# Performance work log

Measured on AMD Instinct MI355X. Metric: run time of the kernel, lower is better.

## Reference

```python
import jax, jax.numpy as jnp
import numpy as np


def _xavier(key, shape):
    fan_out, fan_in = shape[0], shape[1]
    lim = np.sqrt(6.0 / (fan_in + fan_out)).astype(np.float32)
    return jax.random.uniform(key, shape, jnp.float32, -lim, lim)


def setup_inputs() -> dict:
    key = jax.random.key(0)
    ks = jax.random.split(key, 28)
    B, D, G, ND = 16384, 32, 6, 8
    V_user, V_item, V_gender, V_age, V_occ, V_genre = 1000000, 100000, 2, 7, 21, 19
    H1, H2 = 128, 64
    deep_in = 6 * D + ND  # 200
    return {
        "user_id": jax.random.randint(ks[0], (B,), 0, V_user),
        "item_id": jax.random.randint(ks[1], (B,), 0, V_item),
        "user_gender": jax.random.randint(ks[2], (B,), 0, V_gender),
        "user_age": jax.random.randint(ks[3], (B,), 0, V_age),
        "user_occupation": jax.random.randint(ks[4], (B,), 0, V_occ),
        "item_genre_ids": jax.random.randint(ks[5], (B, G), 0, V_genre),
        "item_genre_mask": jax.random.randint(ks[6], (B, G), 0, 2).astype(jnp.float32),
        "dense_features": jax.random.normal(ks[7], (B, ND), jnp.float32),
        # first-order (1-dim) embedding tables
        "fo_user": _xavier(ks[8], (V_user, 1)),
        "fo_item": _xavier(ks[9], (V_item, 1)),
        "fo_gender": _xavier(ks[10], (V_gender, 1)),
        "fo_age": _xavier(ks[11], (V_age, 1)),
        "fo_occ": _xavier(ks[12], (V_occ, 1)),
        "fo_genre": _xavier(ks[13], (V_genre, 1)),
        # second-order / deep embedding tables
        "emb_user": _xavier(ks[14], (V_user, D)),
        "emb_item": _xavier(ks[15], (V_item, D)),
        "emb_gender": _xavier(ks[16], (V_gender, D)),
        "emb_age": _xavier(ks[17], (V_age, D)),
        "emb_occ": _xavier(ks[18], (V_occ, D)),
        "emb_genre": _xavier(ks[19], (V_genre, D)),
        # dense linear + deep MLP
        "dense_W": _xavier(ks[20], (1, ND)),
        "dense_b": jnp.zeros((1,), jnp.float32),
        "W1": _xavier(ks[21], (H1, deep_in)),
        "b1": jnp.zeros((H1,), jnp.float32),
        "W2": _xavier(ks[22], (H2, H1)),
        "b2": jnp.zeros((H2,), jnp.float32),
        "Wout": _xavier(ks[23], (1, H2)),
        "bout": jnp.zeros((1,), jnp.float32),
    }


def _pool(table, ids, mask):
    # masked mean-pool over the genre list axis
    e = table[ids]                       # [B, G, d]
    m = mask[..., None]                  # [B, G, 1]
    denom = jnp.clip(m.sum(axis=1), 1.0)  # [B, 1]
    return (e * m).sum(axis=1) / denom   # [B, d]


def reference(user_id, item_id, user_gender, user_age, user_occupation,
              item_genre_ids, item_genre_mask, dense_features,
              fo_user, fo_item, fo_gender, fo_age, fo_occ, fo_genre,
              emb_user, emb_item, emb_gender, emb_age, emb_occ, emb_genre,
              dense_W, dense_b, W1, b1, W2, b2, Wout, bout):
    # FM first order: sum of 1-dim gathers + pooled genre + dense linear -> [B,1]
    first = (fo_user[user_id] + fo_item[item_id] + fo_gender[user_gender]
             + fo_age[user_age] + fo_occ[user_occupation]
             + _pool(fo_genre, item_genre_ids, item_genre_mask)
             + dense_features @ dense_W.T + dense_b)
    # FM second order: stack field embeddings [B, 6, D]
    x = jnp.stack([emb_user[user_id], emb_item[item_id], emb_gender[user_gender],
                   emb_age[user_age], emb_occ[user_occupation],
                   _pool(emb_genre, item_genre_ids, item_genre_mask)], axis=1)
    s = x.sum(axis=1)                                   # [B, D]
    second = 0.5 * (s * s - (x * x).sum(axis=1)).sum(axis=1, keepdims=True)  # [B,1]
    # deep part (dropout is identity in eval mode)
    deep_in = jnp.concatenate([x.reshape(x.shape[0], -1), dense_features], axis=1)
    h = jax.nn.relu(deep_in @ W1.T + b1)
    h = jax.nn.relu(h @ W2.T + b2)
    deep = h @ Wout.T + bout                            # [B,1]
    return (first + second + deep).squeeze(1)           # [B]
```

## Files before the change

### kernel.cpp

```cpp
#include <hip/hip_runtime.h>


typedef float v2f __attribute__((ext_vector_type(2)));
static __device__ __forceinline__ v2f bc2(float x) { v2f r; r.x = x; r.y = x; return r; }
static __device__ __forceinline__ float relu1(float x) { return fmaxf(x, 0.f); }

#define ROWS_PER_BLOCK 16
#define ROWS_PER_WAVE 4
#define DI_STRIDE 204
#define H1_STRIDE 132

__global__ void pack_weights(const float* __restrict__ W1, const float* __restrict__ W2,
                             float4* __restrict__ W1p, float4* __restrict__ W2p) {
    const int idx = blockIdx.x * blockDim.x + threadIdx.x;
    if (idx < 6400) {
        const int s = idx & 1, jp = (idx >> 1) & 15, k4 = (idx >> 5) % 50, w = idx / 1600;
        const int j0 = w * 32 + 2 * jp, c = 4 * k4 + 2 * s;
        W1p[idx] = make_float4(W1[j0 * 200 + c],     W1[(j0 + 1) * 200 + c],
                               W1[j0 * 200 + c + 1], W1[(j0 + 1) * 200 + c + 1]);
    }
    if (idx < 2048) {
        const int s = idx & 1, jp = (idx >> 1) & 7, k4 = (idx >> 4) & 31, w = idx >> 9;
        const int j0 = w * 16 + 2 * jp, c = 4 * k4 + 2 * s;
        W2p[idx] = make_float4(W2[j0 * 128 + c],     W2[(j0 + 1) * 128 + c],
                               W2[j0 * 128 + c + 1], W2[(j0 + 1) * 128 + c + 1]);
    }
}

__global__ __launch_bounds__(256) void deepfm_kernel(
    const int* __restrict__ user_id, const int* __restrict__ item_id,
    const int* __restrict__ gender_, const int* __restrict__ age_,
    const int* __restrict__ occ_, const int* __restrict__ genre_ids,
    const float* __restrict__ genre_mask, const float* __restrict__ dense,
    const float* __restrict__ fo_user, const float* __restrict__ fo_item,
    const float* __restrict__ fo_gender, const float* __restrict__ fo_age,
    const float* __restrict__ fo_occ, const float* __restrict__ fo_genre,
    const float* __restrict__ emb_user, const float* __restrict__ emb_item,
    const float* __restrict__ emb_gender, const float* __restrict__ emb_age,
    const float* __restrict__ emb_occ, const float* __restrict__ emb_genre,
    const float* __restrict__ dense_W, const float* __restrict__ dense_b,
    const float4* __restrict__ W1p, const float* __restrict__ b1,
    const float4* __restrict__ W2p, const float* __restrict__ b2,
    const float* __restrict__ Wout, const float* __restrict__ bout,
    float* __restrict__ out, int B)
{
    __shared__ float lds_di[ROWS_PER_BLOCK][DI_STRIDE];
    __shared__ float lds_rs[ROWS_PER_BLOCK];
    __shared__ float lds_part[ROWS_PER_BLOCK][4];

    const int tid = threadIdx.x;
    const int wid = tid >> 6;
    const int lane = tid & 63;
    const int blockRow0 = blockIdx.x * ROWS_PER_BLOCK;

    {
        const int rowBase = blockRow0 + wid * ROWS_PER_WAVE;
        int uid[ROWS_PER_WAVE], iid[ROWS_PER_WAVE], gg[ROWS_PER_WAVE],
            aa[ROWS_PER_WAVE], oo[ROWS_PER_WAVE];
        #pragma unroll
        for (int r = 0; r < ROWS_PER_WAVE; ++r) {
            int row = rowBase + r; if (row >= B) row = B - 1;
            uid[r] = user_id[row]; iid[r] = item_id[row];
            gg[r] = gender_[row];  aa[r] = age_[row];  oo[r] = occ_[row];
        }

        #pragma unroll
        for (int r = 0; r < ROWS_PER_WAVE; ++r) {
            int row = rowBase + r; if (row >= B) row = B - 1;
            const int ri = wid * ROWS_PER_WAVE + r;

            int gid[6]; float mk[6]; float msum = 0.f;
            #pragma unroll
            for (int t = 0; t < 6; ++t) {
                gid[t] = genre_ids[row * 6 + t];
                mk[t]  = genre_mask[row * 6 + t];
                msum  += mk[t];
            }
            const float inv_den = 1.0f / fmaxf(msum, 1.0f);

            float pe_sum = 0.f, pe_sq = 0.f;
            {
                float v = (lane < 32) ? emb_user[(size_t)uid[r] * 32 + lane]
                                      : emb_item[(size_t)iid[r] * 32 + (lane - 32)];
                lds_di[ri][lane] = v;
                pe_sum += v; pe_sq += v * v;
            }
            {
                float v = (lane < 32) ? emb_gender[gg[r] * 32 + lane]
                                      : emb_age[aa[r] * 32 + (lane - 32)];
                lds_di[ri][64 + lane] = v;
                pe_sum += v; pe_sq += v * v;
            }
            {
                float v;
                if (lane < 32) {
                    v = emb_occ[oo[r] * 32 + lane];
                } else {
                    const int d = lane - 32;
                    float s = 0.f;
                    #pragma unroll
                    for (int t = 0; t < 6; ++t) s += mk[t] * emb_genre[gid[t] * 32 + d];
                    v = s * inv_den;
                }
                lds_di[ri][128 + lane] = v;
                pe_sum += v; pe_sq += v * v;
            }
            if (lane < 8) lds_di[ri][192 + lane] = dense[(size_t)row * 8 + lane];

            float s2 = pe_sum + __shfl_xor(pe_sum, 32);
            float ss = pe_sq  + __shfl_xor(pe_sq, 32);
            float t2 = 0.5f * (s2 * s2 - ss);
            #pragma unroll
            for (int off = 16; off >= 1; off >>= 1) t2 += __shfl_xor(t2, off);

            float fo = fo_user[uid[r]] + fo_item[iid[r]] + fo_gender[gg[r]]
                     + fo_age[aa[r]] + fo_occ[oo[r]];
            float fg = 0.f;
            #pragma unroll
            for (int t = 0; t < 6; ++t) fg += mk[t] * fo_genre[gid[t]];
            fo += fg * inv_den;
            float dd = 0.f;
            #pragma unroll
            for (int j = 0; j < 8; ++j) dd += dense[(size_t)row * 8 + j] * dense_W[j];
            fo += dd + dense_b[0];

            if (lane == 0) lds_rs[ri] = fo + t2;
        }
    }
    __syncthreads();

    const int jp1 = lane & 15;
    const int rh  = lane >> 4;

    v2f acc[ROWS_PER_WAVE];
    #pragma unroll
    for (int r = 0; r < ROWS_PER_WAVE; ++r) acc[r] = bc2(0.f);

    {
        const float4* __restrict__ W1b = W1p + wid * 1600;
        const float4* __restrict__ dv = reinterpret_cast<const float4*>(&lds_di[0][0]);

        for (int k4 = 0; k4 < 50; ++k4) {
            const float4 wa = W1b[(k4 * 16 + jp1) * 2 + 0];
            const float4 wb = W1b[(k4 * 16 + jp1) * 2 + 1];
            const v2f w0 = { wa.x, wa.y }, w1 = { wa.z, wa.w };
            const v2f w2 = { wb.x, wb.y }, w3 = { wb.z, wb.w };
            #pragma unroll
            for (int r = 0; r < ROWS_PER_WAVE; ++r) {
                const float4 a = dv[(rh + 4 * r) * 51 + k4];
                acc[r] = __builtin_elementwise_fma(w0, bc2(a.x), acc[r]);
                acc[r] = __builtin_elementwise_fma(w1, bc2(a.y), acc[r]);
                acc[r] = __builtin_elementwise_fma(w2, bc2(a.z), acc[r]);
                acc[r] = __builtin_elementwise_fma(w3, bc2(a.w), acc[r]);
            }
        }
    }
    __syncthreads();

    float* __restrict__ h1b = &lds_di[0][0];
    {
        const int j0 = wid * 32 + 2 * jp1;
        const float2 bb = *reinterpret_cast<const float2*>(b1 + j0);
        #pragma unroll
        for (int r = 0; r < ROWS_PER_WAVE; ++r) {
            const int row = rh + 4 * r;
            reinterpret_cast<float2*>(h1b)[(row * H1_STRIDE + j0) >> 1] =
                make_float2(relu1(acc[r].x + bb.x), relu1(acc[r].y + bb.y));
        }
    }
    __syncthreads();

    const int jp2 = lane & 7;
    const int rh2 = lane >> 3;

    v2f acc2[2];
    acc2[0] = bc2(0.f); acc2[1] = bc2(0.f);

    {
        const float4* __restrict__ W2b = W2p + wid * 512;
        const float4* __restrict__ h1v = reinterpret_cast<const float4*>(h1b);

        for (int k4 = 0; k4 < 32; ++k4) {
            const float4 wa = W2b[(k4 * 8 + jp2) * 2 + 0];
            const float4 wb = W2b[(k4 * 8 + jp2) * 2 + 1];
            const v2f w0 = { wa.x, wa.y }, w1 = { wa.z, wa.w };
            const v2f w2 = { wb.x, wb.y }, w3 = { wb.z, wb.w };
            #pragma unroll
            for (int t = 0; t < 2; ++t) {
                const float4 h = h1v[(rh2 + 8 * t) * 33 + k4];
                acc2[t] = __builtin_elementwise_fma(w0, bc2(h.x), acc2[t]);
                acc2[t] = __builtin_elementwise_fma(w1, bc2(h.y), acc2[t]);
                acc2[t] = __builtin_elementwise_fma(w2, bc2(h.z), acc2[t]);
                acc2[t] = __builtin_elementwise_fma(w3, bc2(h.w), acc2[t]);
            }
        }
    }

    {
        const int j0 = wid * 16 + 2 * jp2;
        const float2 bb2 = *reinterpret_cast<const float2*>(b2 + j0);
        const float2 wo  = *reinterpret_cast<const float2*>(Wout + j0);
        #pragma unroll
        for (int t = 0; t < 2; ++t) {
            const float h2x = relu1(acc2[t].x + bb2.x);
            const float h2y = relu1(acc2[t].y + bb2.y);
            float v = wo.x * h2x + wo.y * h2y;
            v += __shfl_xor(v, 1); v += __shfl_xor(v, 2); v += __shfl_xor(v, 4);
            if (jp2 == 0) lds_part[rh2 + 8 * t][wid] = v;
        }
    }
    __syncthreads();

    if (tid < ROWS_PER_BLOCK) {
        const int row = blockRow0 + tid;
        if (row < B) {
            const float deep = lds_part[tid][0] + lds_part[tid][1]
                             + lds_part[tid][2] + lds_part[tid][3] + bout[0];
            out[row] = deep + lds_rs[tid];
        }
    }
}

extern "C" void kernel_launch(void* const* d_in, const int* in_sizes, int n_in,
                              void* d_out, int out_size, void* d_ws, size_t ws_size,
                              hipStream_t stream) {
    const int B = in_sizes[0];

    float4* W1p = reinterpret_cast<float4*>(d_ws);
    float4* W2p = reinterpret_cast<float4*>((char*)d_ws + 102400);

    pack_weights<<<25, 256, 0, stream>>>(
        (const float*)d_in[22], (const float*)d_in[24], W1p, W2p);

    const int grid = (B + ROWS_PER_BLOCK - 1) / ROWS_PER_BLOCK;
    deepfm_kernel<<<grid, 256, 0, stream>>>(
        (const int*)d_in[0],  (const int*)d_in[1],  (const int*)d_in[2],
        (const int*)d_in[3],  (const int*)d_in[4],  (const int*)d_in[5],
        (const float*)d_in[6],  (const float*)d_in[7],
        (const float*)d_in[8],  (const float*)d_in[9],  (const float*)d_in[10],
        (const float*)d_in[11], (const float*)d_in[12], (const float*)d_in[13],
        (const float*)d_in[14], (const float*)d_in[15], (const float*)d_in[16],
        (const float*)d_in[17], (const float*)d_in[18], (const float*)d_in[19],
        (const float*)d_in[20], (const float*)d_in[21],
        W1p, (const float*)d_in[23],
        W2p, (const float*)d_in[25],
        (const float*)d_in[26], (const float*)d_in[27],
        (float*)d_out, B);
}
```

Before: 296.1 us.

## Split fused DeepFM kernel into gather/FM kernel and MLP kernel via global scratch

Splits the single fused kernel into a gather+FM kernel (two rows per wave, writing the 200-wide deep input and the FM scalar to workspace) and a separate MLP kernel that reads the deep input directly from global memory instead of LDS. The aim is to decouple latency-bound random embedding gathers from the compute-bound MLP so each runs with better occupancy and parallelism. The cost is an extra global round trip of about 13 MB, plus one more launch, and the MLP now reads its activations through uncoalesced global float4 loads rather than LDS. The MLP loops also gain unroll-2 pragmas.

New measurement: 274.8 us. -7.2%, faster.

```diff
diff --git a/kernel.cpp b/kernel.cpp
--- a/kernel.cpp
+++ b/kernel.cpp
@@ -5,9 +5,6 @@
 static __device__ __forceinline__ v2f bc2(float x) { v2f r; r.x = x; r.y = x; return r; }
 static __device__ __forceinline__ float relu1(float x) { return fmaxf(x, 0.f); }
 
-#define ROWS_PER_BLOCK 16
-#define ROWS_PER_WAVE 4
-#define DI_STRIDE 204
 #define H1_STRIDE 132
 
 __global__ void pack_weights(const float* __restrict__ W1, const float* __restrict__ W2,
@@ -27,7 +24,7 @@
     }
 }
 
-__global__ __launch_bounds__(256) void deepfm_kernel(
+__global__ __launch_bounds__(256) void gather_fm_kernel(
     const int* __restrict__ user_id, const int* __restrict__ item_id,
     const int* __restrict__ gender_, const int* __restrict__ age_,
     const int* __restrict__ occ_, const int* __restrict__ genre_ids,
@@ -39,115 +36,108 @@
     const float* __restrict__ emb_gender, const float* __restrict__ emb_age,
     const float* __restrict__ emb_occ, const float* __restrict__ emb_genre,
     const float* __restrict__ dense_W, const float* __restrict__ dense_b,
+    float* __restrict__ di, float* __restrict__ rs, int B)
+{
+    const int tid = threadIdx.x;
+    const int wid = tid >> 6;
+    const int lane = tid & 63;
+    const int waveG = blockIdx.x * 4 + wid;
+    const int d = lane & 31;
+
+    #pragma unroll
+    for (int r = 0; r < 2; ++r) {
+        int row = waveG * 2 + r; if (row >= B) row = B - 1;
+
+        const int uid = user_id[row], iid = item_id[row];
+        const int gg = gender_[row], aa = age_[row], oo = occ_[row];
+
+        int gid[6]; float mk[6]; float msum = 0.f;
+        #pragma unroll
+        for (int t = 0; t < 6; ++t) {
+            gid[t] = genre_ids[row * 6 + t];
+            mk[t]  = genre_mask[row * 6 + t];
+            msum  += mk[t];
+        }
+        const float inv_den = 1.0f / fmaxf(msum, 1.0f);
+
+        const float v0 = (lane < 32) ? emb_user[(size_t)uid * 32 + d]
+                                     : emb_item[(size_t)iid * 32 + d];
+        const float v1 = (lane < 32) ? emb_gender[gg * 32 + d]
+                                     : emb_age[aa * 32 + d];
+        float v2;
+        if (lane < 32) {
+            v2 = emb_occ[oo * 32 + d];
+        } else {
+            float s = 0.f;
+            #pragma unroll
+            for (int t = 0; t < 6; ++t) s += mk[t] * emb_genre[gid[t] * 32 + d];
+            v2 = s * inv_den;
+        }
+
+        float* __restrict__ dro = di + (size_t)row * 200;
+        dro[lane] = v0;
+        dro[64 + lane] = v1;
+        dro[128 + lane] = v2;
+        if (lane < 8) dro[192 + lane] = dense[(size_t)row * 8 + lane];
+
+        const float pe_sum = v0 + v1 + v2;
+        const float pe_sq  = v0 * v0 + v1 * v1 + v2 * v2;
+        const float s2 = pe_sum + __shfl_xor(pe_sum, 32);
+        const float ss = pe_sq  + __shfl_xor(pe_sq, 32);
+        float t2 = 0.5f * (s2 * s2 - ss);
+        #pragma unroll
+        for (int off = 16; off >= 1; off >>= 1) t2 += __shfl_xor(t2, off);
+
+        float fo = fo_user[uid] + fo_item[iid] + fo_gender[gg]
+                 + fo_age[aa] + fo_occ[oo];
+        float fg = 0.f;
+        #pragma unroll
+        for (int t = 0; t < 6; ++t) fg += mk[t] * fo_genre[gid[t]];
+        fo += fg * inv_den;
+        float dd = 0.f;
+        #pragma unroll
+        for (int j = 0; j < 8; ++j) dd += dense[(size_t)row * 8 + j] * dense_W[j];
+        fo += dd + dense_b[0];
+
+        if (lane == 0) rs[row] = fo + t2;
+    }
+}
+
+__global__ __launch_bounds__(256) void mlp_kernel(
     const float4* __restrict__ W1p, const float* __restrict__ b1,
     const float4* __restrict__ W2p, const float* __restrict__ b2,
     const float* __restrict__ Wout, const float* __restrict__ bout,
+    const float* __restrict__ di, const float* __restrict__ rs,
     float* __restrict__ out, int B)
 {
-    __shared__ float lds_di[ROWS_PER_BLOCK][DI_STRIDE];
-    __shared__ float lds_rs[ROWS_PER_BLOCK];
-    __shared__ float lds_part[ROWS_PER_BLOCK][4];
+    __shared__ float h1s[16][H1_STRIDE];
+    __shared__ float lds_part[16][4];
 
     const int tid = threadIdx.x;
     const int wid = tid >> 6;
     const int lane = tid & 63;
-    const int blockRow0 = blockIdx.x * ROWS_PER_BLOCK;
-
-    {
-        const int rowBase = blockRow0 + wid * ROWS_PER_WAVE;
-        int uid[ROWS_PER_WAVE], iid[ROWS_PER_WAVE], gg[ROWS_PER_WAVE],
-            aa[ROWS_PER_WAVE], oo[ROWS_PER_WAVE];
-        #pragma unroll
-        for (int r = 0; r < ROWS_PER_WAVE; ++r) {
-            int row = rowBase + r; if (row >= B) row = B - 1;
-            uid[r] = user_id[row]; iid[r] = item_id[row];
-            gg[r] = gender_[row];  aa[r] = age_[row];  oo[r] = occ_[row];
-        }
-
-        #pragma unroll
-        for (int r = 0; r < ROWS_PER_WAVE; ++r) {
-            int row = rowBase + r; if (row >= B) row = B - 1;
-            const int ri = wid * ROWS_PER_WAVE + r;
-
-            int gid[6]; float mk[6]; float msum = 0.f;
-            #pragma unroll
-            for (int t = 0; t < 6; ++t) {
-                gid[t] = genre_ids[row * 6 + t];
-                mk[t]  = genre_mask[row * 6 + t];
-                msum  += mk[t];
-            }
-            const float inv_den = 1.0f / fmaxf(msum, 1.0f);
-
-            float pe_sum = 0.f, pe_sq = 0.f;
-            {
-                float v = (lane < 32) ? emb_user[(size_t)uid[r] * 32 + lane]
-                                      : emb_item[(size_t)iid[r] * 32 + (lane - 32)];
-                lds_di[ri][lane] = v;
-                pe_sum += v; pe_sq += v * v;
-            }
-            {
-                float v = (lane < 32) ? emb_gender[gg[r] * 32 + lane]
-                                      : emb_age[aa[r] * 32 + (lane - 32)];
-                lds_di[ri][64 + lane] = v;
-                pe_sum += v; pe_sq += v * v;
-            }
-            {
-                float v;
-                if (lane < 32) {
-                    v = emb_occ[oo[r] * 32 + lane];
-                } else {
-                    const int d = lane - 32;
-                    float s = 0.f;
-                    #pragma unroll
-                    for (int t = 0; t < 6; ++t) s += mk[t] * emb_genre[gid[t] * 32 + d];
-                    v = s * inv_den;
-                }
-                lds_di[ri][128 + lane] = v;
-                pe_sum += v; pe_sq += v * v;
-            }
-            if (lane < 8) lds_di[ri][192 + lane] = dense[(size_t)row * 8 + lane];
-
-            float s2 = pe_sum + __shfl_xor(pe_sum, 32);
-            float ss = pe_sq  + __shfl_xor(pe_sq, 32);
-            float t2 = 0.5f * (s2 * s2 - ss);
-            #pragma unroll
-            for (int off = 16; off >= 1; off >>= 1) t2 += __shfl_xor(t2, off);
-
-            float fo = fo_user[uid[r]] + fo_item[iid[r]] + fo_gender[gg[r]]
-                     + fo_age[aa[r]] + fo_occ[oo[r]];
-            float fg = 0.f;
-            #pragma unroll
-            for (int t = 0; t < 6; ++t) fg += mk[t] * fo_genre[gid[t]];
-            fo += fg * inv_den;
-            float dd = 0.f;
-            #pragma unroll
-            for (int j = 0; j < 8; ++j) dd += dense[(size_t)row * 8 + j] * dense_W[j];
-            fo += dd + dense_b[0];
-
-            if (lane == 0) lds_rs[ri] = fo + t2;
-        }
-    }
-    __syncthreads();
+    const int row0 = blockIdx.x * 16;
 
     const int jp1 = lane & 15;
     const int rh  = lane >> 4;
 
-    v2f acc[ROWS_PER_WAVE];
+    v2f acc[4];
     #pragma unroll
-    for (int r = 0; r < ROWS_PER_WAVE; ++r) acc[r] = bc2(0.f);
+    for (int r = 0; r < 4; ++r) acc[r] = bc2(0.f);
 
     {
         const float4* __restrict__ W1b = W1p + wid * 1600;
-        const float4* __restrict__ dv = reinterpret_cast<const float4*>(&lds_di[0][0]);
-
+        const float4* __restrict__ dg = reinterpret_cast<const float4*>(di);
+
+        #pragma unroll 2
         for (int k4 = 0; k4 < 50; ++k4) {
             const float4 wa = W1b[(k4 * 16 + jp1) * 2 + 0];
             const float4 wb = W1b[(k4 * 16 + jp1) * 2 + 1];
             const v2f w0 = { wa.x, wa.y }, w1 = { wa.z, wa.w };
             const v2f w2 = { wb.x, wb.y }, w3 = { wb.z, wb.w };
             #pragma unroll
-            for (int r = 0; r < ROWS_PER_WAVE; ++r) {
-                const float4 a = dv[(rh + 4 * r) * 51 + k4];
+            for (int r = 0; r < 4; ++r) {
+                const float4 a = dg[(size_t)(row0 + rh + 4 * r) * 50 + k4];
                 acc[r] = __builtin_elementwise_fma(w0, bc2(a.x), acc[r]);
                 acc[r] = __builtin_elementwise_fma(w1, bc2(a.y), acc[r]);
                 acc[r] = __builtin_elementwise_fma(w2, bc2(a.z), acc[r]);
@@ -155,16 +145,14 @@
             }
         }
     }
-    __syncthreads();
-
-    float* __restrict__ h1b = &lds_di[0][0];
+
     {
         const int j0 = wid * 32 + 2 * jp1;
         const float2 bb = *reinterpret_cast<const float2*>(b1 + j0);
         #pragma unroll
-        for (int r = 0; r < ROWS_PER_WAVE; ++r) {
+        for (int r = 0; r < 4; ++r) {
             const int row = rh + 4 * r;
-            reinterpret_cast<float2*>(h1b)[(row * H1_STRIDE + j0) >> 1] =
+            *reinterpret_cast<float2*>(&h1s[row][j0]) =
                 make_float2(relu1(acc[r].x + bb.x), relu1(acc[r].y + bb.y));
         }
     }
@@ -178,8 +166,8 @@
 
     {
         const float4* __restrict__ W2b = W2p + wid * 512;
-        const float4* __restrict__ h1v = reinterpret_cast<const float4*>(h1b);
-
+
+        #pragma unroll 2
         for (int k4 = 0; k4 < 32; ++k4) {
             const float4 wa = W2b[(k4 * 8 + jp2) * 2 + 0];
             const float4 wb = W2b[(k4 * 8 + jp2) * 2 + 1];
@@ -187,7 +175,7 @@
             const v2f w2 = { wb.x, wb.y }, w3 = { wb.z, wb.w };
             #pragma unroll
             for (int t = 0; t < 2; ++t) {
-                const float4 h = h1v[(rh2 + 8 * t) * 33 + k4];
+                const float4 h = *reinterpret_cast<const float4*>(&h1s[rh2 + 8 * t][k4 * 4]);
                 acc2[t] = __builtin_elementwise_fma(w0, bc2(h.x), acc2[t]);
                 acc2[t] = __builtin_elementwise_fma(w1, bc2(h.y), acc2[t]);
                 acc2[t] = __builtin_elementwise_fma(w2, bc2(h.z), acc2[t]);
@@ -211,12 +199,12 @@
     }
     __syncthreads();
 
-    if (tid < ROWS_PER_BLOCK) {
-        const int row = blockRow0 + tid;
+    if (tid < 16) {
+        const int row = row0 + tid;
         if (row < B) {
             const float deep = lds_part[tid][0] + lds_part[tid][1]
                              + lds_part[tid][2] + lds_part[tid][3] + bout[0];
-            out[row] = deep + lds_rs[tid];
+            out[row] = deep + rs[row];
         }
     }
 }
@@ -228,12 +216,14 @@
 
     float4* W1p = reinterpret_cast<float4*>(d_ws);
     float4* W2p = reinterpret_cast<float4*>((char*)d_ws + 102400);
+    float*  di  = reinterpret_cast<float*>((char*)d_ws + 262144);
+    float*  rs  = reinterpret_cast<float*>((char*)d_ws + 262144 + (size_t)B * 800);
 
     pack_weights<<<25, 256, 0, stream>>>(
         (const float*)d_in[22], (const float*)d_in[24], W1p, W2p);
 
-    const int grid = (B + ROWS_PER_BLOCK - 1) / ROWS_PER_BLOCK;
-    deepfm_kernel<<<grid, 256, 0, stream>>>(
+    const int gatherBlocks = (B + 7) / 8;
+    gather_fm_kernel<<<gatherBlocks, 256, 0, stream>>>(
         (const int*)d_in[0],  (const int*)d_in[1],  (const int*)d_in[2],
         (const int*)d_in[3],  (const int*)d_in[4],  (const int*)d_in[5],
         (const float*)d_in[6],  (const float*)d_in[7],
@@ -242,8 +232,12 @@
         (const float*)d_in[14], (const float*)d_in[15], (const float*)d_in[16],
         (const float*)d_in[17], (const float*)d_in[18], (const float*)d_in[19],
         (const float*)d_in[20], (const float*)d_in[21],
+        di, rs, B);
+
+    const int mlpBlocks = (B + 15) / 16;
+    mlp_kernel<<<mlpBlocks, 256, 0, stream>>>(
         W1p, (const float*)d_in[23],
         W2p, (const float*)d_in[25],
         (const float*)d_in[26], (const float*)d_in[27],
-        (float*)d_out, B);
-}
+        di, rs, (float*)d_out, B);
+}
```

## Double block to 32 rows and 8 waves, halving per-wave MLP output slice

Applied to the files above, without the earlier changes.

Each block now handles 32 rows with 512 threads (8 waves). Each wave owns 16 H1 and 8 H2 output columns across 32 rows instead of 32 and 16 columns across 16 rows, and the packed weight layout is changed to match. The aim is to reuse each weight load across more rows and halve weight traffic per output row. The gather loop now loads indices per row without unrolling, which may cut register pressure but loses the overlap of index loads. Larger blocks also change occupancy and LDS use per block.

Result: slower. 306.3 us (+3.4%).

```diff
diff --git a/kernel.cpp b/kernel.cpp
--- a/kernel.cpp
+++ b/kernel.cpp
@@ -5,8 +5,7 @@
 static __device__ __forceinline__ v2f bc2(float x) { v2f r; r.x = x; r.y = x; return r; }
 static __device__ __forceinline__ float relu1(float x) { return fmaxf(x, 0.f); }
 
-#define ROWS_PER_BLOCK 16
-#define ROWS_PER_WAVE 4
+#define ROWS_PER_BLOCK 32
 #define DI_STRIDE 204
 #define H1_STRIDE 132
 
@@ -14,20 +13,20 @@
                              float4* __restrict__ W1p, float4* __restrict__ W2p) {
     const int idx = blockIdx.x * blockDim.x + threadIdx.x;
     if (idx < 6400) {
-        const int s = idx & 1, jp = (idx >> 1) & 15, k4 = (idx >> 5) % 50, w = idx / 1600;
-        const int j0 = w * 32 + 2 * jp, c = 4 * k4 + 2 * s;
+        const int s = idx & 1, jp = (idx >> 1) & 7, k4 = (idx >> 4) % 50, g = idx / 800;
+        const int j0 = g * 16 + 2 * jp, c = 4 * k4 + 2 * s;
         W1p[idx] = make_float4(W1[j0 * 200 + c],     W1[(j0 + 1) * 200 + c],
                                W1[j0 * 200 + c + 1], W1[(j0 + 1) * 200 + c + 1]);
     }
     if (idx < 2048) {
-        const int s = idx & 1, jp = (idx >> 1) & 7, k4 = (idx >> 4) & 31, w = idx >> 9;
-        const int j0 = w * 16 + 2 * jp, c = 4 * k4 + 2 * s;
+        const int s = idx & 1, jp = (idx >> 1) & 3, k4 = (idx >> 3) & 31, g = idx >> 8;
+        const int j0 = g * 8 + 2 * jp, c = 4 * k4 + 2 * s;
         W2p[idx] = make_float4(W2[j0 * 128 + c],     W2[(j0 + 1) * 128 + c],
                                W2[j0 * 128 + c + 1], W2[(j0 + 1) * 128 + c + 1]);
     }
 }
 
-__global__ __launch_bounds__(256) void deepfm_kernel(
+__global__ __launch_bounds__(512) void deepfm_kernel(
     const int* __restrict__ user_id, const int* __restrict__ item_id,
     const int* __restrict__ gender_, const int* __restrict__ age_,
     const int* __restrict__ occ_, const int* __restrict__ genre_ids,
@@ -46,7 +45,7 @@
 {
     __shared__ float lds_di[ROWS_PER_BLOCK][DI_STRIDE];
     __shared__ float lds_rs[ROWS_PER_BLOCK];
-    __shared__ float lds_part[ROWS_PER_BLOCK][4];
+    __shared__ float lds_part[ROWS_PER_BLOCK][8];
 
     const int tid = threadIdx.x;
     const int wid = tid >> 6;
@@ -54,20 +53,15 @@
     const int blockRow0 = blockIdx.x * ROWS_PER_BLOCK;
 
     {
-        const int rowBase = blockRow0 + wid * ROWS_PER_WAVE;
-        int uid[ROWS_PER_WAVE], iid[ROWS_PER_WAVE], gg[ROWS_PER_WAVE],
-            aa[ROWS_PER_WAVE], oo[ROWS_PER_WAVE];
-        #pragma unroll
-        for (int r = 0; r < ROWS_PER_WAVE; ++r) {
+        const int rowBase = blockRow0 + wid * 4;
+
+        #pragma unroll 1
+        for (int r = 0; r < 4; ++r) {
             int row = rowBase + r; if (row >= B) row = B - 1;
-            uid[r] = user_id[row]; iid[r] = item_id[row];
-            gg[r] = gender_[row];  aa[r] = age_[row];  oo[r] = occ_[row];
-        }
-
-        #pragma unroll
-        for (int r = 0; r < ROWS_PER_WAVE; ++r) {
-            int row = rowBase + r; if (row >= B) row = B - 1;
-            const int ri = wid * ROWS_PER_WAVE + r;
+            const int ri = wid * 4 + r;
+
+            const int uid = user_id[row], iid = item_id[row];
+            const int gg = gender_[row], aa = age_[row], oo = occ_[row];
 
             int gid[6]; float mk[6]; float msum = 0.f;
             #pragma unroll
@@ -80,21 +74,21 @@
 
             float pe_sum = 0.f, pe_sq = 0.f;
             {
-                float v = (lane < 32) ? emb_user[(size_t)uid[r] * 32 + lane]
-                                      : emb_item[(size_t)iid[r] * 32 + (lane - 32)];
+                float v = (lane < 32) ? emb_user[(size_t)uid * 32 + lane]
+                                      : emb_item[(size_t)iid * 32 + (lane - 32)];
                 lds_di[ri][lane] = v;
                 pe_sum += v; pe_sq += v * v;
             }
             {
-                float v = (lane < 32) ? emb_gender[gg[r] * 32 + lane]
-                                      : emb_age[aa[r] * 32 + (lane - 32)];
+                float v = (lane < 32) ? emb_gender[gg * 32 + lane]
+                                      : emb_age[aa * 32 + (lane - 32)];
                 lds_di[ri][64 + lane] = v;
                 pe_sum += v; pe_sq += v * v;
             }
             {
                 float v;
                 if (lane < 32) {
-                    v = emb_occ[oo[r] * 32 + lane];
+                    v = emb_occ[oo * 32 + lane];
                 } else {
                     const int d = lane - 32;
                     float s = 0.f;
@@ -113,8 +107,8 @@
             #pragma unroll
             for (int off = 16; off >= 1; off >>= 1) t2 += __shfl_xor(t2, off);
 
-            float fo = fo_user[uid[r]] + fo_item[iid[r]] + fo_gender[gg[r]]
-                     + fo_age[aa[r]] + fo_occ[oo[r]];
+            float fo = fo_user[uid] + fo_item[iid] + fo_gender[gg]
+                     + fo_age[aa] + fo_occ[oo];
             float fg = 0.f;
             #pragma unroll
             for (int t = 0; t < 6; ++t) fg += mk[t] * fo_genre[gid[t]];
@@ -129,25 +123,25 @@
     }
     __syncthreads();
 
-    const int jp1 = lane & 15;
-    const int rh  = lane >> 4;
-
-    v2f acc[ROWS_PER_WAVE];
+    const int jp1 = lane & 7;
+    const int rh  = lane >> 3;
+
+    v2f acc[4];
     #pragma unroll
-    for (int r = 0; r < ROWS_PER_WAVE; ++r) acc[r] = bc2(0.f);
-
-    {
-        const float4* __restrict__ W1b = W1p + wid * 1600;
+    for (int r = 0; r < 4; ++r) acc[r] = bc2(0.f);
+
+    {
+        const float4* __restrict__ W1b = W1p + wid * 800;
         const float4* __restrict__ dv = reinterpret_cast<const float4*>(&lds_di[0][0]);
 
         for (int k4 = 0; k4 < 50; ++k4) {
-            const float4 wa = W1b[(k4 * 16 + jp1) * 2 + 0];
-            const float4 wb = W1b[(k4 * 16 + jp1) * 2 + 1];
+            const float4 wa = W1b[k4 * 16 + jp1 * 2 + 0];
+            const float4 wb = W1b[k4 * 16 + jp1 * 2 + 1];
             const v2f w0 = { wa.x, wa.y }, w1 = { wa.z, wa.w };
             const v2f w2 = { wb.x, wb.y }, w3 = { wb.z, wb.w };
             #pragma unroll
-            for (int r = 0; r < ROWS_PER_WAVE; ++r) {
-                const float4 a = dv[(rh + 4 * r) * 51 + k4];
+            for (int r = 0; r < 4; ++r) {
+                const float4 a = dv[(rh + 8 * r) * 51 + k4];
                 acc[r] = __builtin_elementwise_fma(w0, bc2(a.x), acc[r]);
                 acc[r] = __builtin_elementwise_fma(w1, bc2(a.y), acc[r]);
                 acc[r] = __builtin_elementwise_fma(w2, bc2(a.z), acc[r]);
@@ -159,35 +153,35 @@
 
     float* __restrict__ h1b = &lds_di[0][0];
     {
-        const int j0 = wid * 32 + 2 * jp1;
+        const int j0 = wid * 16 + 2 * jp1;
         const float2 bb = *reinterpret_cast<const float2*>(b1 + j0);
         #pragma unroll
-        for (int r = 0; r < ROWS_PER_WAVE; ++r) {
-            const int row = rh + 4 * r;
-            reinterpret_cast<float2*>(h1b)[(row * H1_STRIDE + j0) >> 1] =
+        for (int r = 0; r < 4; ++r) {
+            const int row = rh + 8 * r;
+            *reinterpret_cast<float2*>(h1b + row * H1_STRIDE + j0) =
                 make_float2(relu1(acc[r].x + bb.x), relu1(acc[r].y + bb.y));
         }
     }
     __syncthreads();
 
-    const int jp2 = lane & 7;
-    const int rh2 = lane >> 3;
+    const int jp2 = lane & 3;
+    const int rh2 = lane >> 2;
 
     v2f acc2[2];
     acc2[0] = bc2(0.f); acc2[1] = bc2(0.f);
 
     {
-        const float4* __restrict__ W2b = W2p + wid * 512;
+        const float4* __restrict__ W2b = W2p + wid * 256;
         const float4* __restrict__ h1v = reinterpret_cast<const float4*>(h1b);
 
         for (int k4 = 0; k4 < 32; ++k4) {
-            const float4 wa = W2b[(k4 * 8 + jp2) * 2 + 0];
-            const float4 wb = W2b[(k4 * 8 + jp2) * 2 + 1];
+            const float4 wa = W2b[k4 * 8 + jp2 * 2 + 0];
+            const float4 wb = W2b[k4 * 8 + jp2 * 2 + 1];
             const v2f w0 = { wa.x, wa.y }, w1 = { wa.z, wa.w };
             const v2f w2 = { wb.x, wb.y }, w3 = { wb.z, wb.w };
             #pragma unroll
             for (int t = 0; t < 2; ++t) {
-                const float4 h = h1v[(rh2 + 8 * t) * 33 + k4];
+                const float4 h = h1v[(rh2 + 16 * t) * 33 + k4];
                 acc2[t] = __builtin_elementwise_fma(w0, bc2(h.x), acc2[t]);
                 acc2[t] = __builtin_elementwise_fma(w1, bc2(h.y), acc2[t]);
                 acc2[t] = __builtin_elementwise_fma(w2, bc2(h.z), acc2[t]);
@@ -197,7 +191,7 @@
     }
 
     {
-        const int j0 = wid * 16 + 2 * jp2;
+        const int j0 = wid * 8 + 2 * jp2;
         const float2 bb2 = *reinterpret_cast<const float2*>(b2 + j0);
         const float2 wo  = *reinterpret_cast<const float2*>(Wout + j0);
         #pragma unroll
@@ -205,8 +199,8 @@
             const float h2x = relu1(acc2[t].x + bb2.x);
             const float h2y = relu1(acc2[t].y + bb2.y);
             float v = wo.x * h2x + wo.y * h2y;
-            v += __shfl_xor(v, 1); v += __shfl_xor(v, 2); v += __shfl_xor(v, 4);
-            if (jp2 == 0) lds_part[rh2 + 8 * t][wid] = v;
+            v += __shfl_xor(v, 1); v += __shfl_xor(v, 2);
+            if (jp2 == 0) lds_part[rh2 + 16 * t][wid] = v;
         }
     }
     __syncthreads();
@@ -214,8 +208,9 @@
     if (tid < ROWS_PER_BLOCK) {
         const int row = blockRow0 + tid;
         if (row < B) {
-            const float deep = lds_part[tid][0] + lds_part[tid][1]
-                             + lds_part[tid][2] + lds_part[tid][3] + bout[0];
+            float deep = bout[0];
+            #pragma unroll
+            for (int w = 0; w < 8; ++w) deep += lds_part[tid][w];
             out[row] = deep + lds_rs[tid];
         }
     }
@@ -233,7 +228,7 @@
         (const float*)d_in[22], (const float*)d_in[24], W1p, W2p);
 
     const int grid = (B + ROWS_PER_BLOCK - 1) / ROWS_PER_BLOCK;
-    deepfm_kernel<<<grid, 256, 0, stream>>>(
+    deepfm_kernel<<<grid, 512, 0, stream>>>(
         (const int*)d_in[0],  (const int*)d_in[1],  (const int*)d_in[2],
         (const int*)d_in[3],  (const int*)d_in[4],  (const int*)d_in[5],
         (const float*)d_in[6],  (const float*)d_in[7],
```
